# Kernel optimization log

Measured on AMD Instinct MI355X. Metric: run time of the kernel, lower is better.

## Reference

```python
import jax, jax.numpy as jnp
import numpy as np
from jax import lax

B, P, N, D, L, H = 16, 8192, 1024, 384, 12, 6
HD = D // H
K_NEI = 5          # HomogeneityLoss k
KL_RATIO = 1.0


def setup_inputs() -> dict:
    key = jax.random.key(0)
    ks = jax.random.split(key, 10)
    s = lambda i, shape, sc=0.02: (jax.random.normal(ks[i], shape, jnp.float32) * sc)
    return dict(
        pts=jax.random.normal(ks[0], (B, P, 3), jnp.float32),
        grid=jax.random.normal(ks[1], (B, N, 3), jnp.float32),
        embed_w=s(2, (3, D), 0.1),
        proj_w=s(3, (D, 3), 0.1),
        ln1_w=jnp.ones((L, D)), ln1_b=jnp.zeros((L, D)),
        qkv_w=s(4, (L, D, 3 * D)), qkv_b=jnp.zeros((L, 3 * D)),
        attn_w=s(5, (L, D, D)), attn_b=jnp.zeros((L, D)),
        ln2_w=jnp.ones((L, D)), ln2_b=jnp.zeros((L, D)),
        mlp_w1=s(6, (L, D, 4 * D)), mlp_b1=jnp.zeros((L, 4 * D)),
        mlp_w2=s(7, (L, 4 * D, D)), mlp_b2=jnp.zeros((L, D)),
    )


def _ln(x, w, b):
    m = jnp.mean(x, -1, keepdims=True)
    v = jnp.var(x, -1, keepdims=True)
    return (x - m) * lax.rsqrt(v + 1e-5) * w + b


def _transformer(x, params):
    def layer(x, p):
        l1w, l1b, qw, qb, aw, ab, l2w, l2b, m1w, m1b, m2w, m2b = p
        h = _ln(x, l1w, l1b)
        qkv = h @ qw + qb                                   # [B,N,3D]
        q, k, v = jnp.split(qkv, 3, axis=-1)
        rs = lambda t: t.reshape(B, N, H, HD).transpose(0, 2, 1, 3)  # [B,H,N,HD]
        q, k, v = rs(q), rs(k), rs(v)
        att = jax.nn.softmax(jnp.einsum('bhnd,bhmd->bhnm', q, k) / np.sqrt(HD), axis=-1)
        o = jnp.einsum('bhnm,bhmd->bhnd', att, v).transpose(0, 2, 1, 3).reshape(B, N, D)
        x = x + (o @ aw + ab)
        h = _ln(x, l2w, l2b)
        x = x + (jax.nn.gelu(h @ m1w + m1b) @ m2w + m2b)
        return x, None
    x, _ = lax.scan(layer, x, params)
    return x


def _fps(points):  # points: [P,3] -> N int32 indices (farthest point sampling)
    def body(carry, _):
        dists, last = carry
        d = jnp.sum((points - points[last]) ** 2, axis=-1)
        dists = jnp.minimum(dists, d)
        return (dists, jnp.argmax(dists).astype(jnp.int32)), last
    init = (jnp.full((points.shape[0],), 1e10, points.dtype), jnp.int32(0))
    (_, _), idxs = lax.scan(body, init, None, length=N)
    return idxs


def reference(pts, grid, embed_w, proj_w, ln1_w, ln1_b, qkv_w, qkv_b,
              attn_w, attn_b, ln2_w, ln2_b, mlp_w1, mlp_b1, mlp_w2, mlp_b2):
    params = (ln1_w, ln1_b, qkv_w, qkv_b, attn_w, attn_b,
              ln2_w, ln2_b, mlp_w1, mlp_b1, mlp_w2, mlp_b2)
    x = grid @ embed_w                                      # [B,N,D]
    x = _transformer(x, params)
    pred = x @ proj_w                                       # [B,N,3]

    # FPS centers from the raw point cloud
    idxs = jax.vmap(_fps)(pts)                              # [B,N]
    centers = jnp.take_along_axis(pts, idxs[..., None], axis=1)  # [B,N,3]

    # Chamfer L1 (symmetric mean of nearest-neighbor L2 norms)
    d = jnp.linalg.norm(pred[:, :, None, :] - centers[:, None, :, :], axis=-1)  # [B,N,N]
    rec = 0.5 * (d.min(axis=2).mean(axis=1) + d.min(axis=1).mean(axis=1))       # [B]

    # Homogeneity: mean dist of K_NEI nearest neighbors -> softmax -> KL(q||p)
    dd = jnp.linalg.norm(pred[:, :, None, :] - pred[:, None, :, :], axis=-1)    # [B,N,N]
    neg_vals, _ = lax.top_k(-dd, K_NEI + 1)                 # smallest K+1 dists
    mean_d = (-neg_vals[..., 1:]).mean(axis=-1)             # drop self -> [B,N]
    logp = jax.nn.log_softmax(mean_d, axis=-1)
    q = 1.0 / N
    kl = jnp.sum(q * (jnp.log(q) - logp), axis=-1)          # [B]

    return rec.mean(), KL_RATIO * kl.mean()
```

## Files before the change

### kernel.cpp

```cpp
#include <hip/hip_runtime.h>
#include <math.h>

#define B_   16
#define P_   8192
#define N_   1024
#define D_   384
#define L_   12
#define H_   6
#define HD_  64
#define M_   (B_*N_)
#define DQKV_ (3*D_)
#define DH_   (4*D_)

typedef unsigned short ushort_t;
typedef __attribute__((ext_vector_type(8))) short short8;
typedef __attribute__((ext_vector_type(4))) float floatx4;

__device__ __forceinline__ ushort_t f2bf(float f) {
    unsigned u = __float_as_uint(f);
    unsigned rounding = 0x7fffu + ((u >> 16) & 1u);
    return (ushort_t)((u + rounding) >> 16);
}
__device__ __forceinline__ float bf2f(ushort_t u) {
    return __uint_as_float(((unsigned)u) << 16);
}

__global__ __launch_bounds__(D_) void embed_kernel(const float* __restrict__ g,
                                                   const float* __restrict__ ew,
                                                   float* __restrict__ X) {
    int m = blockIdx.x;
    int d = threadIdx.x;
    float g0 = g[m*3+0], g1 = g[m*3+1], g2 = g[m*3+2];
    X[(size_t)m*D_ + d] = g0*ew[0*D_+d] + g1*ew[1*D_+d] + g2*ew[2*D_+d];
}

__global__ __launch_bounds__(256) void transcast_kernel(const float* __restrict__ W,
                                                        ushort_t* __restrict__ Wt,
                                                        int K, int Nc) {
    __shared__ float t[32][33];
    const float* Wl = W + (size_t)blockIdx.z*K*Nc;
    ushort_t* Wtl = Wt + (size_t)blockIdx.z*K*Nc;
    int n0 = blockIdx.x*32, k0 = blockIdx.y*32;
    int tx = threadIdx.x & 31, ty = threadIdx.x >> 5;
#pragma unroll
    for (int j = 0; j < 32; j += 8)
        t[ty+j][tx] = Wl[(size_t)(k0+ty+j)*Nc + n0+tx];
    __syncthreads();
#pragma unroll
    for (int j = 0; j < 32; j += 8)
        Wtl[(size_t)(n0+ty+j)*K + k0+tx] = f2bf(t[tx][ty+j]);
}

__global__ __launch_bounds__(256) void ln_kernel(const float* __restrict__ Xin,
                                                 const float* __restrict__ w,
                                                 const float* __restrict__ bvec,
                                                 ushort_t* __restrict__ out) {
    int wid = threadIdx.x >> 6, lane = threadIdx.x & 63;
    int row = blockIdx.x*4 + wid;
    const float* xr = Xin + (size_t)row*D_;
    float v[6];
#pragma unroll
    for (int i = 0; i < 6; i++) v[i] = xr[lane + i*64];
    float s = 0.f;
#pragma unroll
    for (int i = 0; i < 6; i++) s += v[i];
#pragma unroll
    for (int off = 32; off; off >>= 1) s += __shfl_xor(s, off, 64);
    float mean = s * (1.0f/(float)D_);
    float vs = 0.f;
#pragma unroll
    for (int i = 0; i < 6; i++) { float d = v[i]-mean; vs += d*d; }
#pragma unroll
    for (int off = 32; off; off >>= 1) vs += __shfl_xor(vs, off, 64);
    float var = vs * (1.0f/(float)D_);
    float rstd = 1.0f / sqrtf(var + 1e-5f);
    ushort_t* orow = out + (size_t)row*D_;
#pragma unroll
    for (int i = 0; i < 6; i++) {
        int e = lane + i*64;
        orow[e] = f2bf((v[i]-mean)*rstd*w[e] + bvec[e]);
    }
}

__device__ __forceinline__ float gelu_f(float x) {
    const float c = 0.7978845608028654f;
    float x3 = x*x*x;
    return 0.5f*x*(1.0f + tanhf(c*(x + 0.044715f*x3)));
}

template<int EPI>
__global__ __launch_bounds__(256) void mfma_gemm(const ushort_t* __restrict__ A,
                                                 const ushort_t* __restrict__ Wt,
                                                 const float* __restrict__ bias,
                                                 void* __restrict__ Cout,
                                                 ushort_t* __restrict__ VT,
                                                 int K, int Nc) {
    __shared__ __attribute__((aligned(16))) ushort_t smem[2*128*32];
    ushort_t* smA = smem;
    ushort_t* smB = smem + 128*32;
    int tid = threadIdx.x;
    int lane = tid & 63, w = tid >> 6;
    int wm = w >> 1, wn = w & 1;
    int L = lane & 15, G = lane >> 4;
    int rowBase = blockIdx.y * 128, colBase = blockIdx.x * 128;

    floatx4 acc[4][4];
#pragma unroll
    for (int i = 0; i < 4; i++)
#pragma unroll
        for (int j = 0; j < 4; j++) acc[i][j] = (floatx4){0.f,0.f,0.f,0.f};

    int sr = tid >> 2;
    int kc = tid & 3;
    const ushort_t* Ag = A  + (size_t)(rowBase + sr)*K + kc*8;
    const ushort_t* Bg = Wt + (size_t)(colBase + sr)*K + kc*8;
    size_t step64 = (size_t)64*K;

    short8 ra0, ra1, rb0, rb1;
    ra0 = *(const short8*)(Ag);
    ra1 = *(const short8*)(Ag + step64);
    rb0 = *(const short8*)(Bg);
    rb1 = *(const short8*)(Bg + step64);

    for (int k0 = 0; k0 < K; k0 += 32) {
        __syncthreads();
        *(short8*)(smA + sr*32 + kc*8)        = ra0;
        *(short8*)(smA + (64+sr)*32 + kc*8)   = ra1;
        *(short8*)(smB + sr*32 + kc*8)        = rb0;
        *(short8*)(smB + (64+sr)*32 + kc*8)   = rb1;
        __syncthreads();
        if (k0 + 32 < K) {
            ra0 = *(const short8*)(Ag + k0 + 32);
            ra1 = *(const short8*)(Ag + step64 + k0 + 32);
            rb0 = *(const short8*)(Bg + k0 + 32);
            rb1 = *(const short8*)(Bg + step64 + k0 + 32);
        }
        short8 af[4], bfr[4];
#pragma unroll
        for (int t = 0; t < 4; t++) {
            af[t]  = *(const short8*)(smA + (wm*64 + t*16 + L)*32 + G*8);
            bfr[t] = *(const short8*)(smB + (wn*64 + t*16 + L)*32 + G*8);
        }
#pragma unroll
        for (int mt = 0; mt < 4; mt++)
#pragma unroll
            for (int nt = 0; nt < 4; nt++)
                acc[mt][nt] = __builtin_amdgcn_mfma_f32_16x16x32_bf16(
                    af[mt], bfr[nt], acc[mt][nt], 0, 0, 0);
        __syncthreads();
    }

    __syncthreads();

    if (EPI == 3 && colBase >= 2*D_) {
        int cBase = colBase + wn*64 + L;
        int rBase = rowBase + wm*64 + G*4;
#pragma unroll
        for (int nt = 0; nt < 4; nt++) {
            int col = cBase + nt*16;
            float bv = bias[col];
            int hh = (col - 2*D_) >> 6, d = (col - 2*D_) & 63;
#pragma unroll
            for (int mt = 0; mt < 4; mt++) {
#pragma unroll
                for (int r = 0; r < 4; r++) {
                    int row = rBase + mt*16 + r;
                    int b = row >> 10, n = row & 1023;
                    VT[(((size_t)b*H_ + hh)*64 + d)*N_ + n] = f2bf(acc[mt][nt][r] + bv);
                }
            }
        }
    } else if (EPI == 1) {
        float* fs = (float*)smem + w*1024;
        int orow = lane >> 2, c4 = lane & 3;
#pragma unroll
        for (int mt = 0; mt < 4; mt++) {
#pragma unroll
            for (int nt = 0; nt < 4; nt++) {
                float bv = bias[colBase + wn*64 + nt*16 + L];
#pragma unroll
                for (int r = 0; r < 4; r++)
                    fs[(G*4+r)*64 + nt*16 + L] = acc[mt][nt][r] + bv;
            }
            float* og = (float*)Cout + (size_t)(rowBase + wm*64 + mt*16 + orow)*Nc
                        + colBase + wn*64;
#pragma unroll
            for (int kk = 0; kk < 4; kk++) {
                float4 sv = *(float4*)(fs + orow*64 + kk*16 + c4*4);
                float4 gv = *(float4*)(og + kk*16 + c4*4);
                gv.x += sv.x; gv.y += sv.y; gv.z += sv.z; gv.w += sv.w;
                *(float4*)(og + kk*16 + c4*4) = gv;
            }
        }
    } else {
        ushort_t* us = smem + w*1152;
        int orow = lane >> 2, oc = lane & 3;
#pragma unroll
        for (int mt = 0; mt < 4; mt++) {
#pragma unroll
            for (int nt = 0; nt < 4; nt++) {
                float bv = bias[colBase + wn*64 + nt*16 + L];
#pragma unroll
                for (int r = 0; r < 4; r++) {
                    float v = acc[mt][nt][r] + bv;
                    if (EPI == 2) v = gelu_f(v);
                    us[(G*4+r)*72 + nt*16 + L] = f2bf(v);
                }
            }
            short8 o0 = *(short8*)(us + orow*72 + oc*8);
            short8 o1 = *(short8*)(us + orow*72 + 32 + oc*8);
            ushort_t* og = (ushort_t*)Cout + (size_t)(rowBase + wm*64 + mt*16 + orow)*Nc
                           + colBase + wn*64;
            *(short8*)(og + oc*8) = o0;
            *(short8*)(og + 32 + oc*8) = o1;
        }
    }
}

#define LPAD 72
__global__ __launch_bounds__(256) void fattn_kernel(const ushort_t* __restrict__ QKV,
                                                    const ushort_t* __restrict__ VT,
                                                    ushort_t* __restrict__ O) {
    __shared__ __attribute__((aligned(16))) ushort_t Ks[64*LPAD];
    __shared__ __attribute__((aligned(16))) ushort_t Vs[64*LPAD];
    __shared__ __attribute__((aligned(16))) ushort_t Pw[4*16*LPAD];
    int b = blockIdx.z, h = blockIdx.y;
    int qBase = blockIdx.x * 64;
    int tid = threadIdx.x;
    int lane = tid & 63, w = tid >> 6;
    int L = lane & 15, G = lane >> 4;

    short8 qf[2];
    {
        const ushort_t* qp = QKV + ((size_t)(b*N_ + qBase + w*16 + L))*DQKV_ + h*HD_ + G*8;
        qf[0] = *(const short8*)(qp);
        qf[1] = *(const short8*)(qp + 32);
    }

    floatx4 oacc[4];
#pragma unroll
    for (int nt = 0; nt < 4; nt++) oacc[nt] = (floatx4){0.f,0.f,0.f,0.f};
    float mrow[4], lrow[4];
#pragma unroll
    for (int r = 0; r < 4; r++) { mrow[r] = -3.0e38f; lrow[r] = 0.f; }

    ushort_t* pw = Pw + w*16*LPAD;
    const ushort_t* Kbase = QKV + (size_t)b*N_*DQKV_ + D_ + h*HD_;
    const ushort_t* Vbase = VT + ((size_t)b*H_ + h)*64*N_;

    int srow = tid >> 3;
    int dc   = tid & 7;
    const ushort_t* Kg0 = Kbase + (size_t)srow*DQKV_ + dc*8;
    const ushort_t* Kg1 = Kbase + (size_t)(srow+32)*DQKV_ + dc*8;
    const ushort_t* Vg0 = Vbase + (size_t)srow*N_ + dc*8;
    const ushort_t* Vg1 = Vbase + (size_t)(srow+32)*N_ + dc*8;

    short8 rk0, rk1, rv0, rv1;
    rk0 = *(const short8*)(Kg0);
    rk1 = *(const short8*)(Kg1);
    rv0 = *(const short8*)(Vg0);
    rv1 = *(const short8*)(Vg1);

    for (int kt = 0; kt < N_/64; kt++) {
        __syncthreads();
        *(short8*)(Ks + srow*LPAD + dc*8)       = rk0;
        *(short8*)(Ks + (srow+32)*LPAD + dc*8)  = rk1;
        *(short8*)(Vs + srow*LPAD + dc*8)       = rv0;
        *(short8*)(Vs + (srow+32)*LPAD + dc*8)  = rv1;
        __syncthreads();
        if (kt + 1 < N_/64) {
            rk0 = *(const short8*)(Kg0 + (size_t)(kt+1)*64*DQKV_);
            rk1 = *(const short8*)(Kg1 + (size_t)(kt+1)*64*DQKV_);
            rv0 = *(const short8*)(Vg0 + (kt+1)*64);
            rv1 = *(const short8*)(Vg1 + (kt+1)*64);
        }

        floatx4 sc[4];
#pragma unroll
        for (int ct = 0; ct < 4; ct++) sc[ct] = (floatx4){0.f,0.f,0.f,0.f};
#pragma unroll
        for (int ks = 0; ks < 2; ks++)
#pragma unroll
            for (int ct = 0; ct < 4; ct++) {
                short8 bf = *(const short8*)(Ks + (ct*16 + L)*LPAD + ks*32 + G*8);
                sc[ct] = __builtin_amdgcn_mfma_f32_16x16x32_bf16(qf[ks], bf, sc[ct], 0, 0, 0);
            }

        float rmax[4], rsum[4];
#pragma unroll
        for (int r = 0; r < 4; r++) {
#pragma unroll
            for (int ct = 0; ct < 4; ct++) sc[ct][r] *= 0.125f;
            rmax[r] = fmaxf(fmaxf(sc[0][r], sc[1][r]), fmaxf(sc[2][r], sc[3][r]));
        }
#pragma unroll
        for (int off = 1; off < 16; off <<= 1)
#pragma unroll
            for (int r = 0; r < 4; r++) rmax[r] = fmaxf(rmax[r], __shfl_xor(rmax[r], off, 64));
        float corr[4];
#pragma unroll
        for (int r = 0; r < 4; r++) {
            float mn = fmaxf(mrow[r], rmax[r]);
            corr[r] = __expf(mrow[r] - mn);
            mrow[r] = mn;
            rsum[r] = 0.f;
#pragma unroll
            for (int ct = 0; ct < 4; ct++) {
                float p = __expf(sc[ct][r] - mn);
                sc[ct][r] = p;
                rsum[r] += p;
            }
        }
#pragma unroll
        for (int off = 1; off < 16; off <<= 1)
#pragma unroll
            for (int r = 0; r < 4; r++) rsum[r] += __shfl_xor(rsum[r], off, 64);
#pragma unroll
        for (int r = 0; r < 4; r++) lrow[r] = lrow[r]*corr[r] + rsum[r];

#pragma unroll
        for (int ct = 0; ct < 4; ct++)
#pragma unroll
            for (int r = 0; r < 4; r++)
                pw[(G*4 + r)*LPAD + ct*16 + L] = f2bf(sc[ct][r]);
#pragma unroll
        for (int nt = 0; nt < 4; nt++)
#pragma unroll
            for (int r = 0; r < 4; r++) oacc[nt][r] *= corr[r];

#pragma unroll
        for (int ks = 0; ks < 2; ks++) {
            short8 pf = *(const short8*)(pw + L*LPAD + ks*32 + G*8);
#pragma unroll
            for (int nt = 0; nt < 4; nt++) {
                short8 vf = *(const short8*)(Vs + (nt*16 + L)*LPAD + ks*32 + G*8);
                oacc[nt] = __builtin_amdgcn_mfma_f32_16x16x32_bf16(pf, vf, oacc[nt], 0, 0, 0);
            }
        }
    }

    float inv[4];
#pragma unroll
    for (int r = 0; r < 4; r++) inv[r] = 1.0f / lrow[r];
#pragma unroll
    for (int nt = 0; nt < 4; nt++)
#pragma unroll
        for (int r = 0; r < 4; r++)
            pw[(G*4 + r)*LPAD + nt*16 + L] = f2bf(oacc[nt][r]*inv[r]);
    int orow = lane >> 2, oc = lane & 3;
    short8 o0 = *(short8*)(pw + orow*LPAD + oc*8);
    short8 o1 = *(short8*)(pw + orow*LPAD + 32 + oc*8);
    ushort_t* og = O + (size_t)(b*N_ + qBase + w*16 + orow)*D_ + h*HD_;
    *(short8*)(og + oc*8) = o0;
    *(short8*)(og + 32 + oc*8) = o1;
}

__global__ __launch_bounds__(256) void proj_kernel(const float* __restrict__ X,
                                                   const float* __restrict__ pw,
                                                   float* __restrict__ pred) {
    int m = blockIdx.x*256 + threadIdx.x;
    const float* xr = X + (size_t)m*D_;
    float a0 = 0.f, a1 = 0.f, a2 = 0.f;
    for (int k = 0; k < D_; k++) {
        float xv = xr[k];
        a0 += xv*pw[k*3+0]; a1 += xv*pw[k*3+1]; a2 += xv*pw[k*3+2];
    }
    pred[m*3+0] = a0; pred[m*3+1] = a1; pred[m*3+2] = a2;
}

__global__ __launch_bounds__(1024) void fps_kernel(const float* __restrict__ pts,
                                                   float* __restrict__ centers) {
    __shared__ float Lx[P_], Ly[P_], Lz[P_];
    __shared__ unsigned long long slot[2][16];
    int b = blockIdx.x, t = threadIdx.x;
    const float* pb = pts + (size_t)b*P_*3;
    float px[8], py[8], pz[8], dist[8];
#pragma unroll
    for (int j = 0; j < 8; j++) {
        int p = j*1024 + t;
        px[j] = pb[p*3+0]; py[j] = pb[p*3+1]; pz[j] = pb[p*3+2];
        Lx[p] = px[j]; Ly[p] = py[j]; Lz[p] = pz[j];
        dist[j] = 1e10f;
    }
    int wid = t >> 6;
    int winner = 0;
    __syncthreads();
    for (int it = 0; it < N_; it++) {
        float lx = Lx[winner], ly = Ly[winner], lz = Lz[winner];
        if (t == 0) {
            float* c = centers + ((size_t)b*N_ + it)*3;
            c[0] = lx; c[1] = ly; c[2] = lz;
        }
        unsigned long long best = 0ull;
#pragma unroll
        for (int j = 0; j < 8; j++) {
            float dx = __fsub_rn(px[j], lx);
            float dy = __fsub_rn(py[j], ly);
            float dz = __fsub_rn(pz[j], lz);
            float d = __fadd_rn(__fadd_rn(__fmul_rn(dx,dx), __fmul_rn(dy,dy)), __fmul_rn(dz,dz));
            d = fminf(dist[j], d);
            dist[j] = d;
            unsigned long long pk = ((unsigned long long)__float_as_uint(d) << 32)
                                  | (unsigned)(~(unsigned)(j*1024 + t));
            best = (pk > best) ? pk : best;
        }
#pragma unroll
        for (int off = 32; off; off >>= 1) {
            unsigned long long o = __shfl_xor(best, off, 64);
            best = (o > best) ? o : best;
        }
        int par = it & 1;
        if ((t & 63) == 0) slot[par][wid] = best;
        __syncthreads();
        unsigned long long s0, s1, s2, s3, s4, s5, s6, s7;
        s0 = slot[par][0];  s1 = slot[par][1];  s2 = slot[par][2];  s3 = slot[par][3];
        s4 = slot[par][4];  s5 = slot[par][5];  s6 = slot[par][6];  s7 = slot[par][7];
        s0 = (s1 > s0) ? s1 : s0;  s2 = (s3 > s2) ? s3 : s2;
        s4 = (s5 > s4) ? s5 : s4;  s6 = (s7 > s6) ? s7 : s6;
        s0 = (s2 > s0) ? s2 : s0;  s4 = (s6 > s4) ? s6 : s4;
        s0 = (s4 > s0) ? s4 : s0;
        unsigned long long u0, u1, u2, u3, u4, u5, u6, u7;
        u0 = slot[par][8];  u1 = slot[par][9];  u2 = slot[par][10]; u3 = slot[par][11];
        u4 = slot[par][12]; u5 = slot[par][13]; u6 = slot[par][14]; u7 = slot[par][15];
        u0 = (u1 > u0) ? u1 : u0;  u2 = (u3 > u2) ? u3 : u2;
        u4 = (u5 > u4) ? u5 : u4;  u6 = (u7 > u6) ? u7 : u6;
        u0 = (u2 > u0) ? u2 : u0;  u4 = (u6 > u4) ? u6 : u4;
        u0 = (u4 > u0) ? u4 : u0;
        s0 = (u0 > s0) ? u0 : s0;
        winner = (int)(~(unsigned)(s0 & 0xFFFFFFFFull));
    }
}

__global__ __launch_bounds__(256) void nnmin_kernel(const float* __restrict__ Asrc,
                                                    const float* __restrict__ Bsrc,
                                                    float* __restrict__ outmin) {
    int b = blockIdx.y;
    int i = blockIdx.x*256 + threadIdx.x;
    __shared__ float tile[256][3];
    const float* ar = Asrc + ((size_t)b*N_ + i)*3;
    float ax = ar[0], ay = ar[1], az = ar[2];
    float best = 3.0e38f;
    for (int j0 = 0; j0 < N_; j0 += 256) {
        __syncthreads();
        const float* br = Bsrc + ((size_t)b*N_ + j0 + threadIdx.x)*3;
        tile[threadIdx.x][0] = br[0]; tile[threadIdx.x][1] = br[1]; tile[threadIdx.x][2] = br[2];
        __syncthreads();
        for (int j = 0; j < 256; j++) {
            float dx = ax - tile[j][0], dy = ay - tile[j][1], dz = az - tile[j][2];
            float d = dx*dx + dy*dy + dz*dz;
            best = fminf(best, d);
        }
    }
    outmin[(size_t)b*N_ + i] = sqrtf(best);
}

__global__ __launch_bounds__(256) void knn_kernel(const float* __restrict__ Pp,
                                                  float* __restrict__ mean_d) {
    int b = blockIdx.y;
    int i = blockIdx.x*256 + threadIdx.x;
    __shared__ float tile[256][3];
    const float* ar = Pp + ((size_t)b*N_ + i)*3;
    float ax = ar[0], ay = ar[1], az = ar[2];
    float s[6];
#pragma unroll
    for (int q = 0; q < 6; q++) s[q] = 3.0e38f;
    for (int j0 = 0; j0 < N_; j0 += 256) {
        __syncthreads();
        const float* br = Pp + ((size_t)b*N_ + j0 + threadIdx.x)*3;
        tile[threadIdx.x][0] = br[0]; tile[threadIdx.x][1] = br[1]; tile[threadIdx.x][2] = br[2];
        __syncthreads();
        for (int j = 0; j < 256; j++) {
            float dx = ax - tile[j][0], dy = ay - tile[j][1], dz = az - tile[j][2];
            float d = dx*dx + dy*dy + dz*dz;
            if (d < s[5]) {
                s[5] = d;
#pragma unroll
                for (int q = 5; q > 0; q--)
                    if (s[q] < s[q-1]) { float tmp = s[q]; s[q] = s[q-1]; s[q-1] = tmp; }
            }
        }
    }
    float msum = sqrtf(s[1]) + sqrtf(s[2]) + sqrtf(s[3]) + sqrtf(s[4]) + sqrtf(s[5]);
    mean_d[(size_t)b*N_ + i] = msum * 0.2f;
}

__global__ __launch_bounds__(256) void kl_kernel(const float* __restrict__ md,
                                                 float* __restrict__ klb) {
    int b = blockIdx.x, t = threadIdx.x;
    const float* row = md + (size_t)b*N_;
    float v[4];
#pragma unroll
    for (int i = 0; i < 4; i++) v[i] = row[t + i*256];
    float mx = fmaxf(fmaxf(v[0], v[1]), fmaxf(v[2], v[3]));
#pragma unroll
    for (int off = 32; off; off >>= 1) mx = fmaxf(mx, __shfl_xor(mx, off, 64));
    __shared__ float redm[4], rse[4], rsx[4];
    int wid = t >> 6, lane = t & 63;
    if (lane == 0) redm[wid] = mx;
    __syncthreads();
    mx = fmaxf(fmaxf(redm[0], redm[1]), fmaxf(redm[2], redm[3]));
    float se = 0.f, sx = 0.f;
#pragma unroll
    for (int i = 0; i < 4; i++) { se += expf(v[i]-mx); sx += v[i]; }
#pragma unroll
    for (int off = 32; off; off >>= 1) { se += __shfl_xor(se, off, 64); sx += __shfl_xor(sx, off, 64); }
    if (lane == 0) { rse[wid] = se; rsx[wid] = sx; }
    __syncthreads();
    if (t == 0) {
        float SE = rse[0]+rse[1]+rse[2]+rse[3];
        float SX = rsx[0]+rsx[1]+rsx[2]+rsx[3];
        klb[b] = mx + logf(SE) - SX*(1.0f/(float)N_) - logf((float)N_);
    }
}

__global__ __launch_bounds__(256) void final_kernel(const float* __restrict__ rma,
                                                    const float* __restrict__ rmb,
                                                    const float* __restrict__ klb,
                                                    float* __restrict__ out) {
    int t = threadIdx.x;
    float s = 0.f;
    for (int i = t; i < B_*N_; i += 256) s += rma[i] + rmb[i];
#pragma unroll
    for (int off = 32; off; off >>= 1) s += __shfl_xor(s, off, 64);
    __shared__ float red[4];
    int wid = t >> 6, lane = t & 63;
    if (lane == 0) red[wid] = s;
    __syncthreads();
    if (t == 0) {
        float S = red[0]+red[1]+red[2]+red[3];
        out[0] = 0.5f*S/(float)(B_*N_);
        float K = 0.f;
        for (int b = 0; b < B_; b++) K += klb[b];
        out[1] = K/(float)B_;
    }
}

extern "C" void kernel_launch(void* const* d_in, const int* in_sizes, int n_in,
                              void* d_out, int out_size, void* d_ws, size_t ws_size,
                              hipStream_t stream) {
    (void)in_sizes; (void)n_in; (void)out_size; (void)ws_size;
    const float* pts     = (const float*)d_in[0];
    const float* grid    = (const float*)d_in[1];
    const float* embed_w = (const float*)d_in[2];
    const float* proj_w  = (const float*)d_in[3];
    const float* ln1_w   = (const float*)d_in[4];
    const float* ln1_b   = (const float*)d_in[5];
    const float* qkv_w   = (const float*)d_in[6];
    const float* qkv_b   = (const float*)d_in[7];
    const float* attn_w  = (const float*)d_in[8];
    const float* attn_b  = (const float*)d_in[9];
    const float* ln2_w   = (const float*)d_in[10];
    const float* ln2_b   = (const float*)d_in[11];
    const float* mlp_w1  = (const float*)d_in[12];
    const float* mlp_b1  = (const float*)d_in[13];
    const float* mlp_w2  = (const float*)d_in[14];
    const float* mlp_b2  = (const float*)d_in[15];
    float* out = (float*)d_out;

    float*    X     = (float*)d_ws;
    ushort_t* Hb16  = (ushort_t*)(X + (size_t)M_*D_);
    ushort_t* BIG16 = Hb16 + (size_t)M_*D_;
    ushort_t* VT    = BIG16 + (size_t)M_*DH_;
    ushort_t* WQ    = VT  + (size_t)B_*H_*HD_*N_;
    ushort_t* WA    = WQ  + (size_t)L_*DQKV_*D_;
    ushort_t* WM1   = WA  + (size_t)L_*D_*D_;
    ushort_t* WM2   = WM1 + (size_t)L_*DH_*D_;
    float*    PRED  = (float*)(WM2 + (size_t)L_*D_*DH_);
    float*    CENT  = PRED + (size_t)M_*3;
    float*    RMA   = CENT + (size_t)B_*N_*3;
    float*    RMB   = RMA  + (size_t)B_*N_;
    float*    MEAND = RMB  + (size_t)B_*N_;
    float*    KLB   = MEAND + (size_t)B_*N_;

    transcast_kernel<<<dim3(DQKV_/32, D_/32,  L_), 256, 0, stream>>>(qkv_w,  WQ,  D_,  DQKV_);
    transcast_kernel<<<dim3(D_/32,    D_/32,  L_), 256, 0, stream>>>(attn_w, WA,  D_,  D_);
    transcast_kernel<<<dim3(DH_/32,   D_/32,  L_), 256, 0, stream>>>(mlp_w1, WM1, D_,  DH_);
    transcast_kernel<<<dim3(D_/32,    DH_/32, L_), 256, 0, stream>>>(mlp_w2, WM2, DH_, D_);

    fps_kernel<<<B_, 1024, 0, stream>>>(pts, CENT);

    embed_kernel<<<M_, D_, 0, stream>>>(grid, embed_w, X);

    for (int l = 0; l < L_; l++) {
        ln_kernel<<<M_/4, 256, 0, stream>>>(X, ln1_w + l*D_, ln1_b + l*D_, Hb16);
        mfma_gemm<3><<<dim3(DQKV_/128, M_/128), 256, 0, stream>>>(
            Hb16, WQ + (size_t)l*DQKV_*D_, qkv_b + l*DQKV_, BIG16, VT, D_, DQKV_);
        fattn_kernel<<<dim3(N_/64, H_, B_), 256, 0, stream>>>(BIG16, VT, Hb16);
        mfma_gemm<1><<<dim3(D_/128, M_/128), 256, 0, stream>>>(
            Hb16, WA + (size_t)l*D_*D_, attn_b + l*D_, X, nullptr, D_, D_);
        ln_kernel<<<M_/4, 256, 0, stream>>>(X, ln2_w + l*D_, ln2_b + l*D_, Hb16);
        mfma_gemm<2><<<dim3(DH_/128, M_/128), 256, 0, stream>>>(
            Hb16, WM1 + (size_t)l*DH_*D_, mlp_b1 + l*DH_, BIG16, nullptr, D_, DH_);
        mfma_gemm<1><<<dim3(D_/128, M_/128), 256, 0, stream>>>(
            BIG16, WM2 + (size_t)l*D_*DH_, mlp_b2 + l*D_, X, nullptr, DH_, D_);
    }

    proj_kernel<<<M_/256, 256, 0, stream>>>(X, proj_w, PRED);

    nnmin_kernel<<<dim3(N_/256, B_), 256, 0, stream>>>(PRED, CENT, RMA);
    nnmin_kernel<<<dim3(N_/256, B_), 256, 0, stream>>>(CENT, PRED, RMB);
    knn_kernel<<<dim3(N_/256, B_), 256, 0, stream>>>(PRED, MEAND);
    kl_kernel<<<B_, 256, 0, stream>>>(MEAND, KLB);
    final_kernel<<<1, 256, 0, stream>>>(RMA, RMB, KLB, out);
}
```

Measured before the change: 4.847 ms.

## Shrink FPS block, use scalar argmax scan, and warp-parallelize projection

The FPS kernel now runs 512 threads per batch, each holding 16 points. It tracks the per-thread best with a float compare plus index and packs to 64-bit only once before the wave shuffle. The cross-wave reduction now uses 8 slots combined with shuffles instead of 16 serial LDS loads. The projection kernel assigns one wavefront per row with coalesced loads and a shuffle reduction, replacing one thread per row with strided loads. FPS is a serial 1024-iteration loop on only 16 blocks, so cutting per-iteration sync and reduction cost matters, though fewer threads means more serial work per thread. Ties within a thread keep the lowest j, which matches the previous index-packing order.

```diff
diff --git a/kernel.cpp b/kernel.cpp
--- a/kernel.cpp
+++ b/kernel.cpp
@@ -13,6 +13,7 @@
 #define DH_   (4*D_)
 
 typedef unsigned short ushort_t;
+typedef unsigned long long u64_t;
 typedef __attribute__((ext_vector_type(8))) short short8;
 typedef __attribute__((ext_vector_type(4))) float floatx4;
 
@@ -358,31 +359,42 @@
 __global__ __launch_bounds__(256) void proj_kernel(const float* __restrict__ X,
                                                    const float* __restrict__ pw,
                                                    float* __restrict__ pred) {
-    int m = blockIdx.x*256 + threadIdx.x;
+    int wid = threadIdx.x >> 6, lane = threadIdx.x & 63;
+    int m = blockIdx.x*4 + wid;
     const float* xr = X + (size_t)m*D_;
     float a0 = 0.f, a1 = 0.f, a2 = 0.f;
-    for (int k = 0; k < D_; k++) {
+#pragma unroll
+    for (int i = 0; i < 6; i++) {
+        int k = lane + i*64;
         float xv = xr[k];
         a0 += xv*pw[k*3+0]; a1 += xv*pw[k*3+1]; a2 += xv*pw[k*3+2];
     }
-    pred[m*3+0] = a0; pred[m*3+1] = a1; pred[m*3+2] = a2;
-}
-
-__global__ __launch_bounds__(1024) void fps_kernel(const float* __restrict__ pts,
-                                                   float* __restrict__ centers) {
+#pragma unroll
+    for (int off = 32; off; off >>= 1) {
+        a0 += __shfl_xor(a0, off, 64);
+        a1 += __shfl_xor(a1, off, 64);
+        a2 += __shfl_xor(a2, off, 64);
+    }
+    if (lane == 0) {
+        pred[m*3+0] = a0; pred[m*3+1] = a1; pred[m*3+2] = a2;
+    }
+}
+
+__global__ __launch_bounds__(512) void fps_kernel(const float* __restrict__ pts,
+                                                  float* __restrict__ centers) {
     __shared__ float Lx[P_], Ly[P_], Lz[P_];
-    __shared__ unsigned long long slot[2][16];
+    __shared__ u64_t slot[2][8];
     int b = blockIdx.x, t = threadIdx.x;
     const float* pb = pts + (size_t)b*P_*3;
-    float px[8], py[8], pz[8], dist[8];
-#pragma unroll
-    for (int j = 0; j < 8; j++) {
-        int p = j*1024 + t;
+    float px[16], py[16], pz[16], dist[16];
+#pragma unroll
+    for (int j = 0; j < 16; j++) {
+        int p = j*512 + t;
         px[j] = pb[p*3+0]; py[j] = pb[p*3+1]; pz[j] = pb[p*3+2];
         Lx[p] = px[j]; Ly[p] = py[j]; Lz[p] = pz[j];
         dist[j] = 1e10f;
     }
-    int wid = t >> 6;
+    int wid = t >> 6, lane = t & 63;
     int winner = 0;
     __syncthreads();
     for (int it = 0; it < N_; it++) {
@@ -391,43 +403,36 @@
             float* c = centers + ((size_t)b*N_ + it)*3;
             c[0] = lx; c[1] = ly; c[2] = lz;
         }
-        unsigned long long best = 0ull;
-#pragma unroll
-        for (int j = 0; j < 8; j++) {
+        float bd = -1.0f; int bj = 0;
+#pragma unroll
+        for (int j = 0; j < 16; j++) {
             float dx = __fsub_rn(px[j], lx);
             float dy = __fsub_rn(py[j], ly);
             float dz = __fsub_rn(pz[j], lz);
             float d = __fadd_rn(__fadd_rn(__fmul_rn(dx,dx), __fmul_rn(dy,dy)), __fmul_rn(dz,dz));
             d = fminf(dist[j], d);
             dist[j] = d;
-            unsigned long long pk = ((unsigned long long)__float_as_uint(d) << 32)
-                                  | (unsigned)(~(unsigned)(j*1024 + t));
-            best = (pk > best) ? pk : best;
-        }
+            bool gt = d > bd;
+            bd = gt ? d : bd;
+            bj = gt ? j : bj;
+        }
+        u64_t best = ((u64_t)__float_as_uint(bd) << 32)
+                   | (unsigned)(~(unsigned)(bj*512 + t));
 #pragma unroll
         for (int off = 32; off; off >>= 1) {
-            unsigned long long o = __shfl_xor(best, off, 64);
+            u64_t o = __shfl_xor(best, off, 64);
             best = (o > best) ? o : best;
         }
         int par = it & 1;
-        if ((t & 63) == 0) slot[par][wid] = best;
-        __syncthreads();
-        unsigned long long s0, s1, s2, s3, s4, s5, s6, s7;
-        s0 = slot[par][0];  s1 = slot[par][1];  s2 = slot[par][2];  s3 = slot[par][3];
-        s4 = slot[par][4];  s5 = slot[par][5];  s6 = slot[par][6];  s7 = slot[par][7];
-        s0 = (s1 > s0) ? s1 : s0;  s2 = (s3 > s2) ? s3 : s2;
-        s4 = (s5 > s4) ? s5 : s4;  s6 = (s7 > s6) ? s7 : s6;
-        s0 = (s2 > s0) ? s2 : s0;  s4 = (s6 > s4) ? s6 : s4;
-        s0 = (s4 > s0) ? s4 : s0;
-        unsigned long long u0, u1, u2, u3, u4, u5, u6, u7;
-        u0 = slot[par][8];  u1 = slot[par][9];  u2 = slot[par][10]; u3 = slot[par][11];
-        u4 = slot[par][12]; u5 = slot[par][13]; u6 = slot[par][14]; u7 = slot[par][15];
-        u0 = (u1 > u0) ? u1 : u0;  u2 = (u3 > u2) ? u3 : u2;
-        u4 = (u5 > u4) ? u5 : u4;  u6 = (u7 > u6) ? u7 : u6;
-        u0 = (u2 > u0) ? u2 : u0;  u4 = (u6 > u4) ? u6 : u4;
-        u0 = (u4 > u0) ? u4 : u0;
-        s0 = (u0 > s0) ? u0 : s0;
-        winner = (int)(~(unsigned)(s0 & 0xFFFFFFFFull));
+        if (lane == 0) slot[par][wid] = best;
+        __syncthreads();
+        u64_t v = slot[par][lane & 7];
+#pragma unroll
+        for (int off = 1; off < 8; off <<= 1) {
+            u64_t o = __shfl_xor(v, off, 64);
+            v = (o > v) ? o : v;
+        }
+        winner = (int)(~(unsigned)(v & 0xFFFFFFFFull));
     }
 }
 
@@ -577,7 +582,7 @@
     transcast_kernel<<<dim3(DH_/32,   D_/32,  L_), 256, 0, stream>>>(mlp_w1, WM1, D_,  DH_);
     transcast_kernel<<<dim3(D_/32,    DH_/32, L_), 256, 0, stream>>>(mlp_w2, WM2, DH_, D_);
 
-    fps_kernel<<<B_, 1024, 0, stream>>>(pts, CENT);
+    fps_kernel<<<B_, 512, 0, stream>>>(pts, CENT);
 
     embed_kernel<<<M_, D_, 0, stream>>>(grid, embed_w, X);
 
@@ -595,7 +600,7 @@
             BIG16, WM2 + (size_t)l*D_*DH_, mlp_b2 + l*D_, X, nullptr, DH_, D_);
     }
 
-    proj_kernel<<<M_/256, 256, 0, stream>>>(X, proj_w, PRED);
+    proj_kernel<<<M_/4, 256, 0, stream>>>(X, proj_w, PRED);
 
     nnmin_kernel<<<dim3(N_/256, B_), 256, 0, stream>>>(PRED, CENT, RMA);
     nnmin_kernel<<<dim3(N_/256, B_), 256, 0, stream>>>(CENT, PRED, RMB);
```

After: 4.619 ms. 1.05x faster.
